# Kernel optimization log

Measured on AMD Instinct MI355X. Metric: run time of the kernel, lower is better.

Reference implementation:

```python
import jax, jax.numpy as jnp
import numpy as np
import math

MAX_FREQ = 64
SHIFT = 1


def real_sph_harmonics(theta, phi, max_freq, shift):
    """Fully-normalized real spherical harmonics Y_{|m|+shift, m} for m=-max_freq..max_freq.

    Matches torch module: scipy sph_harm (Condon-Shortley phase included) combined into
    real harmonics, real part taken. Uses stable normalized associated-Legendre
    recurrences so no factorial overflow.
    theta, phi: (..., h, w, 1). Returns (..., h, w, 1, 2*max_freq+1).
    """
    ct = jnp.cos(phi)
    st = jnp.sqrt(jnp.maximum(1.0 - ct * ct, 0.0))  # sin(phi) for phi in [0, pi]
    sqrt2 = math.sqrt(2.0)
    # Pbar_0^0 = sqrt(1/(4*pi))
    pmm = jnp.full(theta.shape, math.sqrt(1.0 / (4.0 * math.pi)), dtype=theta.dtype)
    pos, neg, y0 = [], [], None
    for m in range(max_freq + 1):
        if m > 0:
            # Pbar_m^m = -sqrt((2m+1)/(2m)) * sin(phi) * Pbar_{m-1}^{m-1}  (CS phase)
            pmm = (-math.sqrt((2 * m + 1) / (2 * m))) * st * pmm
        # climb l from m to m+shift via normalized recurrence
        p_lm2, p_lm1 = None, pmm
        l = m
        for _ in range(shift):
            l += 1
            a = math.sqrt((4 * l * l - 1) / (l * l - m * m))
            if p_lm2 is None:
                p = a * ct * p_lm1
            else:
                bb = math.sqrt(((l - 1) ** 2 - m * m) / (4 * (l - 1) ** 2 - 1))
                p = a * (ct * p_lm1 - bb * p_lm2)
            p_lm2, p_lm1 = p_lm1, p
        ybar = p_lm1  # N_{lm} * P_l^m(cos phi) with CS phase, l = m + shift
        if m == 0:
            y0 = ybar
        else:
            # torch module: m>0 even -> +sqrt2*Re(Y), odd -> -sqrt2*Re(Y); mirrored for m<0 with sin
            sgn = sqrt2 if (m % 2 == 0) else -sqrt2
            pos.append(sgn * ybar * jnp.cos(m * theta))
            neg.append(sgn * ybar * jnp.sin(m * theta))
    ys = neg[::-1] + [y0] + pos  # order m = -max_freq .. max_freq
    return jnp.stack(ys, axis=-1)


def setup_inputs() -> dict:
    key = jax.random.key(0)
    k1, k2, k3 = jax.random.split(key, 3)
    x = jax.random.uniform(k1, (4, 128, 256, 1, 2), dtype=jnp.float32)  # (theta, phi)
    n_harm = 2 * MAX_FREQ + 1
    W = jax.random.normal(k2, (1024, n_harm), dtype=jnp.float32) / math.sqrt(n_harm)
    b = jax.random.normal(k3, (1024,), dtype=jnp.float32) * 0.01
    return {"x": x, "W": W, "b": b}


def reference(x, W, b):
    theta = x[..., 0]  # (..., h, w, 1)
    phi = x[..., 1]
    Y = real_sph_harmonics(theta, phi, MAX_FREQ, SHIFT)  # (..., h, w, 1, 2F+1)
    return jnp.einsum('...k,hk->...h', Y, W) + b
```

## Files before the change

### kernel.cpp

```cpp
#include <hip/hip_runtime.h>
#include <math.h>

#define KP 136

typedef short v8s __attribute__((ext_vector_type(8)));
typedef float v4f __attribute__((ext_vector_type(4)));

__device__ __forceinline__ unsigned short bf16_rne(float f, float* back) {
    union { float f; unsigned u; } a; a.f = f;
    unsigned r = a.u + 0x7FFFu + ((a.u >> 16) & 1u);
    unsigned short h = (unsigned short)(r >> 16);
    union { unsigned u; float f; } bb; bb.u = (unsigned)h << 16;
    *back = bb.f;
    return h;
}


__global__ __launch_bounds__(512)
void sph_prep(const float* __restrict__ x, const float* __restrict__ W,
              unsigned short* __restrict__ Yhi, unsigned short* __restrict__ Ylo,
              float* __restrict__ y128,
              unsigned short* __restrict__ Whi, unsigned short* __restrict__ Wlo,
              float* __restrict__ w128c, int P) {
    const int tid = threadIdx.x;
    const int nyb = P >> 7;
    const int b = blockIdx.x;

    if (b < nyb) {
        const int pix = tid & 127;
        const int s   = tid >> 7;
        const int m0  = 16 * s;
        const int p   = b * 128 + pix;
        const float2 tp = *(const float2*)&x[(size_t)p * 2];
        const float theta = tp.x, phi = tp.y;

        const float ct = cosf(phi);
        const float st = sqrtf(fmaxf(1.0f - ct * ct, 0.0f));

        float prod = 1.0f;
        for (int i = 1; i <= m0; ++i) prod *= (2.0f * i + 1.0f) / (2.0f * i);
        const float s2_ = st * st, s4 = s2_ * s2_, s8 = s4 * s4, s16 = s8 * s8;
        float stp = 1.0f;
        for (int i = 0; i < s; ++i) stp *= s16;
        float pm = 0.28209479177387814f * sqrtf(prod) * stp;

        float cm, sm, c1, s1;
        sincosf((float)m0 * theta, &sm, &cm);
        sincosf(theta, &s1, &c1);

        unsigned short ph[16], pl[16], nh[16], nl[16];
        float y128v = 0.0f;

        {
            const float yb = sqrtf(2.0f * m0 + 3.0f) * ct * pm;
            const float val = (s == 0) ? yb
                                       : 1.4142135623730951f * yb * cm;
            float hf, d;
            ph[0] = bf16_rne(val, &hf);
            pl[0] = bf16_rne(val - hf, &d);
        }

        #pragma unroll
        for (int j = 1; j <= 16; ++j) {
            const int m = m0 + j;
            pm *= -sqrtf((2.0f * m + 1.0f) / (2.0f * m)) * st;
            const float cn = cm * c1 - sm * s1;
            const float sn = sm * c1 + cm * s1;
            cm = cn; sm = sn;
            const float yb = sqrtf(2.0f * m + 3.0f) * ct * pm;
            const float t  = (m & 1) ? -1.4142135623730951f : 1.4142135623730951f;
            const float vp = t * yb * cm;
            const float vn = t * yb * sm;
            {
                float hf, d;
                nh[16 - j] = bf16_rne(vn, &hf);
                nl[16 - j] = bf16_rne(vn - hf, &d);
            }
            if (j <= 15) {
                float hf, d;
                ph[j] = bf16_rne(vp, &hf);
                pl[j] = bf16_rne(vp - hf, &d);
            } else if (s == 3) {
                y128v = vp;
            }
        }

        {
            v8s vh, vl;
            #pragma unroll
            for (int e = 0; e < 8; ++e) { vh[e] = (short)ph[e]; vl[e] = (short)pl[e]; }
            *(v8s*)&Yhi[((size_t)(8 + 2 * s) * P + p) * 8] = vh;
            *(v8s*)&Ylo[((size_t)(8 + 2 * s) * P + p) * 8] = vl;
        }
        {
            v8s vh, vl;
            #pragma unroll
            for (int e = 0; e < 8; ++e) { vh[e] = (short)ph[8 + e]; vl[e] = (short)pl[8 + e]; }
            *(v8s*)&Yhi[((size_t)(9 + 2 * s) * P + p) * 8] = vh;
            *(v8s*)&Ylo[((size_t)(9 + 2 * s) * P + p) * 8] = vl;
        }
        {
            v8s vh, vl;
            #pragma unroll
            for (int e = 0; e < 8; ++e) { vh[e] = (short)nh[e]; vl[e] = (short)nl[e]; }
            *(v8s*)&Yhi[((size_t)(6 - 2 * s) * P + p) * 8] = vh;
            *(v8s*)&Ylo[((size_t)(6 - 2 * s) * P + p) * 8] = vl;
        }
        {
            v8s vh, vl;
            #pragma unroll
            for (int e = 0; e < 8; ++e) { vh[e] = (short)nh[8 + e]; vl[e] = (short)nl[8 + e]; }
            *(v8s*)&Yhi[((size_t)(7 - 2 * s) * P + p) * 8] = vh;
            *(v8s*)&Ylo[((size_t)(7 - 2 * s) * P + p) * 8] = vl;
        }
        if (s == 3) y128[p] = y128v;
    } else {
        const int idx = (b - nyb) * 512 + tid;
        const int c = idx >> 10;
        const int h = idx & 1023;
        const float* wrow = W + (size_t)h * 129 + c * 8;
        v8s vh, vl;
        #pragma unroll
        for (int e = 0; e < 8; ++e) {
            const float w = wrow[e];
            float hf, d;
            vh[e] = (short)bf16_rne(w, &hf);
            vl[e] = (short)bf16_rne(w - hf, &d);
        }
        *(v8s*)&Whi[((size_t)c * 1024 + h) * 8] = vh;
        *(v8s*)&Wlo[((size_t)c * 1024 + h) * 8] = vl;
        if (idx < 1024) w128c[idx] = W[(size_t)idx * 129 + 128];
    }
}

__global__ __launch_bounds__(256, 4)
void sph_gemm(const unsigned short* __restrict__ Yhi, const unsigned short* __restrict__ Ylo,
              const float* __restrict__ y128,
              const unsigned short* __restrict__ Whi, const unsigned short* __restrict__ Wlo,
              const float* __restrict__ w128c, const float* __restrict__ bias,
              float* __restrict__ out, int P) {
    const int tid  = threadIdx.x;
    const int lane = tid & 63;
    const int wn   = tid >> 6;
    const int l16  = lane & 15;
    const int quad = lane >> 4;
    const int p0 = blockIdx.x * 64;
    const int h0 = blockIdx.y * 128;

    v4f acc[4][2];
    #pragma unroll
    for (int mt = 0; mt < 4; ++mt)
        #pragma unroll
        for (int tn = 0; tn < 2; ++tn)
            acc[mt][tn] = (v4f){0.f, 0.f, 0.f, 0.f};

    #pragma unroll
    for (int ks = 0; ks < 4; ++ks) {
        const int c = ks * 4 + quad;
        v8s ah[4], al[4], bh[2], bl[2];
        #pragma unroll
        for (int mt = 0; mt < 4; ++mt) {
            const size_t ai = ((size_t)c * P + (p0 + mt * 16 + l16)) * 8;
            ah[mt] = *(const v8s*)&Yhi[ai];
            al[mt] = *(const v8s*)&Ylo[ai];
        }
        #pragma unroll
        for (int tn = 0; tn < 2; ++tn) {
            const size_t bi = ((size_t)c * 1024 + (h0 + wn * 32 + tn * 16 + l16)) * 8;
            bh[tn] = *(const v8s*)&Whi[bi];
            bl[tn] = *(const v8s*)&Wlo[bi];
        }
        #pragma unroll
        for (int mt = 0; mt < 4; ++mt)
            #pragma unroll
            for (int tn = 0; tn < 2; ++tn) {
                acc[mt][tn] = __builtin_amdgcn_mfma_f32_16x16x32_bf16(ah[mt], bh[tn], acc[mt][tn], 0, 0, 0);
                acc[mt][tn] = __builtin_amdgcn_mfma_f32_16x16x32_bf16(ah[mt], bl[tn], acc[mt][tn], 0, 0, 0);
                acc[mt][tn] = __builtin_amdgcn_mfma_f32_16x16x32_bf16(al[mt], bh[tn], acc[mt][tn], 0, 0, 0);
            }
    }

    #pragma unroll
    for (int tn = 0; tn < 2; ++tn) {
        const int hc = wn * 32 + tn * 16 + l16;
        const float bv = bias[h0 + hc];
        const float wv = w128c[h0 + hc];
        #pragma unroll
        for (int mt = 0; mt < 4; ++mt) {
            const v4f yv = *(const v4f*)&y128[p0 + mt * 16 + quad * 4];
            #pragma unroll
            for (int i = 0; i < 4; ++i) {
                const int row = mt * 16 + quad * 4 + i;
                out[(size_t)(p0 + row) * 1024 + (h0 + hc)] = acc[mt][tn][i] + bv + yv[i] * wv;
            }
        }
    }
}

__global__ __launch_bounds__(512, 2)
void sph_mfma(const float* __restrict__ x, const float* __restrict__ W,
              const float* __restrict__ bias, float* __restrict__ out) {
    __shared__ alignas(16) unsigned short Yhi[128 * KP];
    __shared__ alignas(16) unsigned short Ylo[128 * KP];
    __shared__ alignas(16) unsigned short Whi[128 * KP];
    __shared__ alignas(16) unsigned short Wlo[128 * KP];
    __shared__ float y128[128];
    __shared__ float w128[128];

    const int tid = threadIdx.x;
    const int p0 = blockIdx.x * 128;
    const int h0 = blockIdx.y * 128;

    {
        const int r  = tid >> 2;
        const int cp = tid & 3;
        const float* wrow = W + (size_t)(h0 + r) * 129;
        #pragma unroll
        for (int i = 0; i < 33; ++i) {
            const int k = cp + 4 * i;
            if (k < 128) {
                const float w = wrow[k];
                float hf;
                Whi[r * KP + k] = bf16_rne(w, &hf);
                float dummy;
                Wlo[r * KP + k] = bf16_rne(w - hf, &dummy);
            } else if (k == 128) {
                w128[r] = wrow[128];
            }
        }
    }

    {
        const int pix = tid & 127;
        const int s   = tid >> 7;
        const int m0  = 16 * s;
        const float2 tp = *(const float2*)&x[(size_t)(p0 + pix) * 2];
        const float theta = tp.x, phi = tp.y;

        const float ct = cosf(phi);
        const float st = sqrtf(fmaxf(1.0f - ct * ct, 0.0f));

        float prod = 1.0f;
        for (int i = 1; i <= m0; ++i) prod *= (2.0f * i + 1.0f) / (2.0f * i);
        const float s2 = st * st, s4 = s2 * s2, s8 = s4 * s4, s16 = s8 * s8;
        float stp = 1.0f;
        for (int i = 0; i < s; ++i) stp *= s16;
        float pm = 0.28209479177387814f * sqrtf(prod) * stp;

        float cm, sm, c1, s1;
        sincosf((float)m0 * theta, &sm, &cm);
        sincosf(theta, &s1, &c1);

        if (s == 0) {
            const float y0 = 1.7320508075688772f * ct * pm;
            float hf, d;
            Yhi[pix * KP + 64] = bf16_rne(y0, &hf);
            Ylo[pix * KP + 64] = bf16_rne(y0 - hf, &d);
        }

        #pragma unroll
        for (int j = 1; j <= 16; ++j) {
            const int m = m0 + j;
            pm *= -sqrtf((2.0f * m + 1.0f) / (2.0f * m)) * st;
            const float cn = cm * c1 - sm * s1;
            const float sn = sm * c1 + cm * s1;
            cm = cn; sm = sn;
            const float yb = sqrtf(2.0f * m + 3.0f) * ct * pm;
            const float t  = (m & 1) ? -1.4142135623730951f : 1.4142135623730951f;
            const float vp = t * yb * cm;
            const float vn = t * yb * sm;
            {
                float hf, d;
                const int kn = 64 - m;
                Yhi[pix * KP + kn] = bf16_rne(vn, &hf);
                Ylo[pix * KP + kn] = bf16_rne(vn - hf, &d);
            }
            const int kp = 64 + m;
            if (kp < 128) {
                float hf, d;
                Yhi[pix * KP + kp] = bf16_rne(vp, &hf);
                Ylo[pix * KP + kp] = bf16_rne(vp - hf, &d);
            } else {
                y128[pix] = vp;
            }
        }
    }
    __syncthreads();

    const int lane = tid & 63;
    const int wid  = tid >> 6;
    const int wm   = wid & 1;
    const int wn   = wid >> 1;
    const int l16  = lane & 15;
    const int quad = lane >> 4;

    const int arow0 = wm * 64 + l16;
    const int brow0 = wn * 32 + l16;

    v4f acc[4][2];
    #pragma unroll
    for (int mt = 0; mt < 4; ++mt)
        #pragma unroll
        for (int tn = 0; tn < 2; ++tn)
            acc[mt][tn] = (v4f){0.f, 0.f, 0.f, 0.f};

    #pragma unroll
    for (int ks = 0; ks < 4; ++ks) {
        const int ko = ks * 32 + quad * 8;
        v8s ah[4], al[4], bh[2], bl[2];
        #pragma unroll
        for (int mt = 0; mt < 4; ++mt) {
            ah[mt] = *(const v8s*)&Yhi[(arow0 + mt * 16) * KP + ko];
            al[mt] = *(const v8s*)&Ylo[(arow0 + mt * 16) * KP + ko];
        }
        #pragma unroll
        for (int tn = 0; tn < 2; ++tn) {
            bh[tn] = *(const v8s*)&Whi[(brow0 + tn * 16) * KP + ko];
            bl[tn] = *(const v8s*)&Wlo[(brow0 + tn * 16) * KP + ko];
        }
        #pragma unroll
        for (int mt = 0; mt < 4; ++mt)
            #pragma unroll
            for (int tn = 0; tn < 2; ++tn) {
                acc[mt][tn] = __builtin_amdgcn_mfma_f32_16x16x32_bf16(ah[mt], bh[tn], acc[mt][tn], 0, 0, 0);
                acc[mt][tn] = __builtin_amdgcn_mfma_f32_16x16x32_bf16(ah[mt], bl[tn], acc[mt][tn], 0, 0, 0);
                acc[mt][tn] = __builtin_amdgcn_mfma_f32_16x16x32_bf16(al[mt], bh[tn], acc[mt][tn], 0, 0, 0);
            }
    }

    #pragma unroll
    for (int tn = 0; tn < 2; ++tn) {
        const int hc = wn * 32 + tn * 16 + l16;
        const float bv = bias[h0 + hc];
        const float wv = w128[hc];
        #pragma unroll
        for (int mt = 0; mt < 4; ++mt) {
            #pragma unroll
            for (int i = 0; i < 4; ++i) {
                const int row = wm * 64 + mt * 16 + quad * 4 + i;
                const float o = acc[mt][tn][i] + bv + y128[row] * wv;
                out[(size_t)(p0 + row) * 1024 + (h0 + hc)] = o;
            }
        }
    }
}

extern "C" void kernel_launch(void* const* d_in, const int* in_sizes, int n_in,
                              void* d_out, int out_size, void* d_ws, size_t ws_size,
                              hipStream_t stream) {
    const float* x = (const float*)d_in[0];
    const float* W = (const float*)d_in[1];
    const float* b = (const float*)d_in[2];
    float* out = (float*)d_out;

    const int P = in_sizes[0] / 2;

    const size_t szY   = (size_t)16 * (size_t)P * 8 * sizeof(unsigned short);
    const size_t szy128 = (size_t)P * sizeof(float);
    const size_t szW   = (size_t)16 * 1024 * 8 * sizeof(unsigned short);
    const size_t szw128 = 1024 * sizeof(float);
    const size_t need = 2 * szY + szy128 + 2 * szW + szw128;

    if (d_ws != nullptr && ws_size >= need) {
        char* base = (char*)d_ws;
        unsigned short* Yhi = (unsigned short*)(base);
        unsigned short* Ylo = (unsigned short*)(base + szY);
        float*          y128 = (float*)(base + 2 * szY);
        unsigned short* Whi = (unsigned short*)(base + 2 * szY + szy128);
        unsigned short* Wlo = (unsigned short*)(base + 2 * szY + szy128 + szW);
        float*          w128c = (float*)(base + 2 * szY + szy128 + 2 * szW);

        const int nyb = P / 128;
        sph_prep<<<dim3(nyb + 32), dim3(512), 0, stream>>>(x, W, Yhi, Ylo, y128, Whi, Wlo, w128c, P);
        sph_gemm<<<dim3(P / 64, 8), dim3(256), 0, stream>>>(Yhi, Ylo, y128, Whi, Wlo, w128c, b, out, P);
    } else {
        dim3 grid(P / 128, 1024 / 128);
        sph_mfma<<<grid, dim3(512), 0, stream>>>(x, W, b, out);
    }
}
```

Baseline: 729.7 us.

## Keep Y fragments resident and loop over all output columns per block

```diff
diff --git a/kernel.cpp b/kernel.cpp
--- a/kernel.cpp
+++ b/kernel.cpp
@@ -133,7 +133,7 @@
     }
 }
 
-__global__ __launch_bounds__(256, 4)
+__global__ __launch_bounds__(256, 3)
 void sph_gemm(const unsigned short* __restrict__ Yhi, const unsigned short* __restrict__ Ylo,
               const float* __restrict__ y128,
               const unsigned short* __restrict__ Whi, const unsigned short* __restrict__ Wlo,
@@ -144,56 +144,83 @@
     const int wn   = tid >> 6;
     const int l16  = lane & 15;
     const int quad = lane >> 4;
-    const int p0 = blockIdx.x * 64;
-    const int h0 = blockIdx.y * 128;
-
-    v4f acc[4][2];
-    #pragma unroll
-    for (int mt = 0; mt < 4; ++mt)
-        #pragma unroll
-        for (int tn = 0; tn < 2; ++tn)
-            acc[mt][tn] = (v4f){0.f, 0.f, 0.f, 0.f};
-
+    const int p0 = blockIdx.x * 32;
+
+    v8s ah[2][4], al[2][4];
     #pragma unroll
     for (int ks = 0; ks < 4; ++ks) {
         const int c = ks * 4 + quad;
-        v8s ah[4], al[4], bh[2], bl[2];
-        #pragma unroll
-        for (int mt = 0; mt < 4; ++mt) {
+        #pragma unroll
+        for (int mt = 0; mt < 2; ++mt) {
             const size_t ai = ((size_t)c * P + (p0 + mt * 16 + l16)) * 8;
-            ah[mt] = *(const v8s*)&Yhi[ai];
-            al[mt] = *(const v8s*)&Ylo[ai];
-        }
+            ah[mt][ks] = *(const v8s*)&Yhi[ai];
+            al[mt][ks] = *(const v8s*)&Ylo[ai];
+        }
+    }
+    v4f yv[2];
+    #pragma unroll
+    for (int mt = 0; mt < 2; ++mt)
+        yv[mt] = *(const v4f*)&y128[p0 + mt * 16 + quad * 4];
+
+    const int bcol = wn * 32 + l16;
+
+    v8s bh[2][2], bl[2][2];
+    #pragma unroll
+    for (int tn = 0; tn < 2; ++tn) {
+        const size_t bi = ((size_t)quad * 1024 + bcol + tn * 16) * 8;
+        bh[0][tn] = *(const v8s*)&Whi[bi];
+        bl[0][tn] = *(const v8s*)&Wlo[bi];
+    }
+
+    #pragma unroll
+    for (int h = 0; h < 8; ++h) {
+        v4f acc[2][2];
+        #pragma unroll
+        for (int mt = 0; mt < 2; ++mt)
+            #pragma unroll
+            for (int tn = 0; tn < 2; ++tn)
+                acc[mt][tn] = (v4f){0.f, 0.f, 0.f, 0.f};
+
+        #pragma unroll
+        for (int ks = 0; ks < 4; ++ks) {
+            const int step = h * 4 + ks;
+            const int par  = step & 1;
+            if (step + 1 < 32) {
+                const int ns  = step + 1;
+                const int nh  = ns >> 2;
+                const int nc  = (ns & 3) * 4 + quad;
+                #pragma unroll
+                for (int tn = 0; tn < 2; ++tn) {
+                    const size_t bi = ((size_t)nc * 1024 + nh * 128 + bcol + tn * 16) * 8;
+                    bh[par ^ 1][tn] = *(const v8s*)&Whi[bi];
+                    bl[par ^ 1][tn] = *(const v8s*)&Wlo[bi];
+                }
+            }
+            #pragma unroll
+            for (int mt = 0; mt < 2; ++mt)
+                #pragma unroll
+                for (int tn = 0; tn < 2; ++tn) {
+                    acc[mt][tn] = __builtin_amdgcn_mfma_f32_16x16x32_bf16(ah[mt][ks], bh[par][tn], acc[mt][tn], 0, 0, 0);
+                    acc[mt][tn] = __builtin_amdgcn_mfma_f32_16x16x32_bf16(ah[mt][ks], bl[par][tn], acc[mt][tn], 0, 0, 0);
+                    acc[mt][tn] = __builtin_amdgcn_mfma_f32_16x16x32_bf16(al[mt][ks], bh[par][tn], acc[mt][tn], 0, 0, 0);
+                }
+        }
+
+        float bv[2], wv[2];
         #pragma unroll
         for (int tn = 0; tn < 2; ++tn) {
-            const size_t bi = ((size_t)c * 1024 + (h0 + wn * 32 + tn * 16 + l16)) * 8;
-            bh[tn] = *(const v8s*)&Whi[bi];
-            bl[tn] = *(const v8s*)&Wlo[bi];
-        }
-        #pragma unroll
-        for (int mt = 0; mt < 4; ++mt)
-            #pragma unroll
-            for (int tn = 0; tn < 2; ++tn) {
-                acc[mt][tn] = __builtin_amdgcn_mfma_f32_16x16x32_bf16(ah[mt], bh[tn], acc[mt][tn], 0, 0, 0);
-                acc[mt][tn] = __builtin_amdgcn_mfma_f32_16x16x32_bf16(ah[mt], bl[tn], acc[mt][tn], 0, 0, 0);
-                acc[mt][tn] = __builtin_amdgcn_mfma_f32_16x16x32_bf16(al[mt], bh[tn], acc[mt][tn], 0, 0, 0);
-            }
-    }
-
-    #pragma unroll
-    for (int tn = 0; tn < 2; ++tn) {
-        const int hc = wn * 32 + tn * 16 + l16;
-        const float bv = bias[h0 + hc];
-        const float wv = w128c[h0 + hc];
-        #pragma unroll
-        for (int mt = 0; mt < 4; ++mt) {
-            const v4f yv = *(const v4f*)&y128[p0 + mt * 16 + quad * 4];
+            bv[tn] = bias[h * 128 + bcol + tn * 16];
+            wv[tn] = w128c[h * 128 + bcol + tn * 16];
+        }
+        #pragma unroll
+        for (int mt = 0; mt < 2; ++mt)
             #pragma unroll
             for (int i = 0; i < 4; ++i) {
                 const int row = mt * 16 + quad * 4 + i;
-                out[(size_t)(p0 + row) * 1024 + (h0 + hc)] = acc[mt][tn][i] + bv + yv[i] * wv;
-            }
-        }
+                float* orow = out + (size_t)(p0 + row) * 1024 + h * 128;
+                orow[bcol]      = acc[mt][0][i] + bv[0] + yv[mt][i] * wv[0];
+                orow[bcol + 16] = acc[mt][1][i] + bv[1] + yv[mt][i] * wv[1];
+            }
     }
 }
 
@@ -372,7 +399,7 @@
 
         const int nyb = P / 128;
         sph_prep<<<dim3(nyb + 32), dim3(512), 0, stream>>>(x, W, Yhi, Ylo, y128, Whi, Wlo, w128c, P);
-        sph_gemm<<<dim3(P / 64, 8), dim3(256), 0, stream>>>(Yhi, Ylo, y128, Whi, Wlo, w128c, b, out, P);
+        sph_gemm<<<dim3(P / 32), dim3(256), 0, stream>>>(Yhi, Ylo, y128, Whi, Wlo, w128c, b, out, P);
     } else {
         dim3 grid(P / 128, 1024 / 128);
         sph_mfma<<<grid, dim3(512), 0, stream>>>(x, W, b, out);
```

New measurement: 631.9 us. 1.15x faster.
